# Kernel tuning notes

Hardware: AMD Instinct MI355X
Metric: run time of the kernel (lower is better)

The kernel has to match this reference:

```python
import jax, jax.numpy as jnp
import numpy as np

DIM = 1024
N_HEADS = 16
N_KV = 4
HEAD_DIM = 64
FFN = 4096
EPS = 1e-6
B, S = 2, 2048
ROPE_BASE = 10000.0


def rmsnorm(x, w, eps=EPS):
    ms = jnp.mean(jnp.square(x), axis=-1, keepdims=True)
    return x * jax.lax.rsqrt(ms + eps) * w


def apply_rotary(x, cos, sin):
    # x: [B,H,S,hd]; cos/sin: [S, hd//2] -> broadcast over B,H
    half = x.shape[-1] // 2
    x1, x2 = x[..., :half], x[..., half:]
    c = cos[None, None, :, :]
    s = sin[None, None, :, :]
    return jnp.concatenate((x1 * c + x2 * s, x2 * c - x1 * s), axis=-1)


def setup_inputs() -> dict:
    key = jax.random.key(0)
    ks = jax.random.split(key, 10)
    w = lambda k, shp: jax.random.normal(k, shp, dtype=jnp.float32) * 0.02
    pos = jnp.arange(S, dtype=jnp.float32)
    inv_freq = 1.0 / (ROPE_BASE ** (jnp.arange(0, HEAD_DIM // 2, dtype=jnp.float32) / (HEAD_DIM // 2)))
    ang = pos[:, None] * inv_freq[None, :]
    return {
        "x": jax.random.normal(ks[0], (B, S, DIM), dtype=jnp.float32),
        "w_norm1": jnp.ones((DIM,), jnp.float32),
        "wq": w(ks[1], (DIM, N_HEADS * HEAD_DIM)),
        "wk": w(ks[2], (DIM, N_KV * HEAD_DIM)),
        "wv": w(ks[3], (DIM, N_KV * HEAD_DIM)),
        "wo": w(ks[4], (N_HEADS * HEAD_DIM, DIM)),
        "attn_scale": jnp.ones((DIM,), jnp.float32),
        "w_norm2": jnp.ones((DIM,), jnp.float32),
        "wg": w(ks[5], (DIM, FFN)),
        "wu": w(ks[6], (DIM, FFN)),
        "wd": w(ks[7], (FFN, DIM)),
        "mlp_scale": jnp.ones((DIM,), jnp.float32),
        "cos": jnp.cos(ang),
        "sin": jnp.sin(ang),
    }


def block_forward(x, w_norm1, wq, wk, wv, wo, attn_scale, w_norm2, wg, wu, wd, mlp_scale, cos, sin):
    b, s, d = x.shape
    # ---- attention sub-block (pre-norm, RoPE, causal GQA SDPA, scaled residual) ----
    xn = rmsnorm(x, w_norm1)
    q = (xn @ wq).reshape(b, s, N_HEADS, HEAD_DIM).transpose(0, 2, 1, 3)  # [B,H,S,hd]
    k = (xn @ wk).reshape(b, s, N_KV, HEAD_DIM).transpose(0, 2, 1, 3)    # [B,KV,S,hd]
    v = (xn @ wv).reshape(b, s, N_KV, HEAD_DIM).transpose(0, 2, 1, 3)
    q = apply_rotary(q, cos, sin)
    k = apply_rotary(k, cos, sin)
    rep = N_HEADS // N_KV
    k = jnp.repeat(k, rep, axis=1)  # GQA expand -> [B,H,S,hd]
    v = jnp.repeat(v, rep, axis=1)
    scale = 1.0 / np.sqrt(HEAD_DIM)
    scores = jnp.einsum("bhqd,bhkd->bhqk", q, k) * scale
    causal = jnp.tril(jnp.ones((s, s), dtype=bool))
    scores = jnp.where(causal[None, None], scores, jnp.finfo(scores.dtype).min)
    probs = jax.nn.softmax(scores, axis=-1)
    attn = jnp.einsum("bhqk,bhkd->bhqd", probs, v)
    attn = attn.transpose(0, 2, 1, 3).reshape(b, s, N_HEADS * HEAD_DIM)
    x = x + (attn @ wo) * attn_scale[None, None, :]
    # ---- MLP sub-block (pre-norm, fused gate/up SwiGLU, down proj, scaled residual) ----
    xn2 = rmsnorm(x, w_norm2)
    hidden = jax.nn.silu(xn2 @ wg) * (xn2 @ wu)  # SwiGLU
    x = x + (hidden @ wd) * mlp_scale[None, None, :]
    return x


def reference(x, w_norm1, wq, wk, wv, wo, attn_scale, w_norm2, wg, wu, wd, mlp_scale, cos, sin):
    return block_forward(x, w_norm1, wq, wk, wv, wo, attn_scale, w_norm2, wg, wu, wd, mlp_scale, cos, sin)
```

## Files before the change

kernel.cpp:

```cpp
#include <hip/hip_runtime.h>
#include <hip/hip_bf16.h>
#include <cstdint>

typedef unsigned short u16;
typedef unsigned int u32;
typedef __attribute__((ext_vector_type(4))) float f32x4;
typedef __attribute__((ext_vector_type(16))) float f32x16;
typedef __attribute__((ext_vector_type(8))) __bf16 bf16x8;

#define NH 16
#define NKV 4
#define SEQ 2048
#define NTOK 4096

__device__ inline u16 f2bf(float f) {
  return __builtin_bit_cast(u16, __float2bfloat16(f));
}
__device__ inline float bf2f(u16 u) {
  return __bfloat162float(__builtin_bit_cast(__hip_bfloat16, u));
}
__device__ inline u32 pk2(float a, float b) {
  return (u32)f2bf(a) | ((u32)f2bf(b) << 16);
}

#define GLDS(gp, lp) __builtin_amdgcn_global_load_lds( \
    (__attribute__((address_space(1))) void*)(gp), \
    (__attribute__((address_space(3))) void*)(lp), 16, 0, 0)

#define VMCNT0 asm volatile("s_waitcnt vmcnt(0)" ::: "memory")

__global__ __launch_bounds__(256) void rmsnorm_kernel(
    const float* __restrict__ x, const float* __restrict__ w,
    u16* __restrict__ out) {
  int row = blockIdx.x;
  int tid = threadIdx.x;
  const float4 v = reinterpret_cast<const float4*>(x + (size_t)row * 1024)[tid];
  float ss = v.x * v.x + v.y * v.y + v.z * v.z + v.w * v.w;
#pragma unroll
  for (int off = 32; off; off >>= 1) ss += __shfl_xor(ss, off);
  __shared__ float red[4];
  int lane = tid & 63, wid = tid >> 6;
  if (lane == 0) red[wid] = ss;
  __syncthreads();
  float tot = red[0] + red[1] + red[2] + red[3];
  float r = rsqrtf(tot * (1.0f / 1024.0f) + 1e-6f);
  const float4 wv = reinterpret_cast<const float4*>(w)[tid];
  ushort4 o;
  o.x = f2bf(v.x * r * wv.x);
  o.y = f2bf(v.y * r * wv.y);
  o.z = f2bf(v.z * r * wv.z);
  o.w = f2bf(v.w * r * wv.w);
  reinterpret_cast<ushort4*>(out + (size_t)row * 1024)[tid] = o;
}

__global__ __launch_bounds__(256) void transpose_cast_kernel(
    const float* __restrict__ src, u16* __restrict__ dst, int K, int N) {
  __shared__ float tile[32][33];
  int n0 = blockIdx.x * 32, k0 = blockIdx.y * 32;
  int tx = threadIdx.x & 31, ty = threadIdx.x >> 5;
#pragma unroll
  for (int i = 0; i < 4; i++)
    tile[ty + i * 8][tx] = src[(size_t)(k0 + ty + i * 8) * N + n0 + tx];
  __syncthreads();
#pragma unroll
  for (int i = 0; i < 4; i++)
    dst[(size_t)(n0 + ty + i * 8) * K + k0 + tx] = f2bf(tile[tx][ty + i * 8]);
}

template <int EP>
__device__ inline void epi_store(float v, size_t idx, int col,
                                 float* __restrict__ outf,
                                 const float* __restrict__ res,
                                 const float* __restrict__ scale,
                                 u16* __restrict__ outb) {
  if (EP == 0) {
    outf[idx] = v;
  } else if (EP == 1) {
    outf[idx] = res[idx] + v * scale[col];
  } else if (EP == 2) {
    outb[idx] = f2bf(v / (1.0f + __expf(-v)));
  } else {
    outb[idx] = f2bf(bf2f(outb[idx]) * v);
  }
}

template <int EP>
__global__ __launch_bounds__(512, 1) void gemmA(
    const u16* __restrict__ A, const u16* __restrict__ Bt,
    int M, int N, int K,
    float* __restrict__ outf, const float* __restrict__ res,
    const float* __restrict__ scale, u16* __restrict__ outb) {
  __shared__ u16 SA[2][256 * 64];
  __shared__ u16 SB[2][256 * 64];
  const int tid = threadIdx.x, lane = tid & 63, w = tid >> 6;
  const int wr = w >> 2, wc = w & 3;
  const int lg = lane >> 4, lc = lane & 15, cx = lc & 7;

  const int nbn = N >> 8;
  const int r8 = blockIdx.x & 7, j = blockIdx.x >> 3;
  const int bm = (((r8 >> 1) << 2) + (j & 3)) << 8;
  const int bn = ((r8 & 1) * (nbn >> 1) + (j >> 2)) << 8;

  const int swrow = lane >> 3;
  const int swcol = (lane & 7) ^ swrow;
  const u16* gA = A + (size_t)(bm + w * 16 + swrow) * K + swcol * 8;
  const u16* gB = Bt + (size_t)(bn + w * 16 + swrow) * K + swcol * 8;

  const int NT = K >> 6;
  f32x4 acc[8][4] = {};

#define SGA(T_) do { int sl_ = (T_) & 1; size_t ko_ = (size_t)(T_) * 64; \
    GLDS(gA + ko_,                    &SA[sl_][(w * 16) * 64]); \
    GLDS(gA + ko_ + (size_t)8 * K,    &SA[sl_][(w * 16 + 8) * 64]); \
    GLDS(gA + ko_ + (size_t)128 * K,  &SA[sl_][(128 + w * 16) * 64]); \
    GLDS(gA + ko_ + (size_t)136 * K,  &SA[sl_][(136 + w * 16) * 64]); } while (0)
#define SGB(T_) do { int sl_ = (T_) & 1; size_t ko_ = (size_t)(T_) * 64; \
    GLDS(gB + ko_,                    &SB[sl_][(w * 16) * 64]); \
    GLDS(gB + ko_ + (size_t)8 * K,    &SB[sl_][(w * 16 + 8) * 64]); \
    GLDS(gB + ko_ + (size_t)128 * K,  &SB[sl_][(128 + w * 16) * 64]); \
    GLDS(gB + ko_ + (size_t)136 * K,  &SB[sl_][(136 + w * 16) * 64]); } while (0)

  SGA(0);
  SGB(0);
  VMCNT0;
  __builtin_amdgcn_s_barrier();

  for (int t = 0; t < NT; ++t) {
    const u16* sa = &SA[t & 1][0];
    const u16* sb = &SB[t & 1][0];
    const bool more = (t + 1 < NT);

    bf16x8 bfr[4][2];
#pragma unroll
    for (int n = 0; n < 4; n++) {
      const int row = wc * 64 + n * 16 + lc;
#pragma unroll
      for (int ks = 0; ks < 2; ks++)
        bfr[n][ks] = *reinterpret_cast<const bf16x8*>(
            &sb[row * 64 + ((((ks << 2) | lg) ^ cx) << 3)]);
    }
    bf16x8 afr[4][2];
#pragma unroll
    for (int i = 0; i < 4; i++) {
      const int row = wr * 128 + i * 16 + lc;
#pragma unroll
      for (int ks = 0; ks < 2; ks++)
        afr[i][ks] = *reinterpret_cast<const bf16x8*>(
            &sa[row * 64 + ((((ks << 2) | lg) ^ cx) << 3)]);
    }
    if (more) SGA(t + 1);
    __builtin_amdgcn_s_setprio(1);
#pragma unroll
    for (int i = 0; i < 4; i++)
#pragma unroll
      for (int n = 0; n < 4; n++) {
        acc[i][n] = __builtin_amdgcn_mfma_f32_16x16x32_bf16(afr[i][0], bfr[n][0], acc[i][n], 0, 0, 0);
        acc[i][n] = __builtin_amdgcn_mfma_f32_16x16x32_bf16(afr[i][1], bfr[n][1], acc[i][n], 0, 0, 0);
      }
    __builtin_amdgcn_s_setprio(0);
#pragma unroll
    for (int i = 0; i < 4; i++) {
      const int row = wr * 128 + 64 + i * 16 + lc;
#pragma unroll
      for (int ks = 0; ks < 2; ks++)
        afr[i][ks] = *reinterpret_cast<const bf16x8*>(
            &sa[row * 64 + ((((ks << 2) | lg) ^ cx) << 3)]);
    }
    if (more) SGB(t + 1);
    __builtin_amdgcn_s_setprio(1);
#pragma unroll
    for (int i = 0; i < 4; i++)
#pragma unroll
      for (int n = 0; n < 4; n++) {
        acc[4 + i][n] = __builtin_amdgcn_mfma_f32_16x16x32_bf16(afr[i][0], bfr[n][0], acc[4 + i][n], 0, 0, 0);
        acc[4 + i][n] = __builtin_amdgcn_mfma_f32_16x16x32_bf16(afr[i][1], bfr[n][1], acc[4 + i][n], 0, 0, 0);
      }
    __builtin_amdgcn_s_setprio(0);
    VMCNT0;
    __builtin_amdgcn_s_barrier();
  }
#undef SGA
#undef SGB

#pragma unroll
  for (int mi = 0; mi < 8; mi++)
#pragma unroll
    for (int ni = 0; ni < 4; ni++)
#pragma unroll
      for (int rg = 0; rg < 4; rg++) {
        const int row = bm + wr * 128 + mi * 16 + lg * 4 + rg;
        const int col = bn + wc * 64 + ni * 16 + lc;
        epi_store<EP>(acc[mi][ni][rg], (size_t)row * N + col, col, outf, res, scale, outb);
      }
}

template <int EP>
__global__ __launch_bounds__(256, 1) void gemmB(
    const u16* __restrict__ A, const u16* __restrict__ Bt,
    int M, int N, int K,
    float* __restrict__ outf, const float* __restrict__ res,
    const float* __restrict__ scale, u16* __restrict__ outb) {
  __shared__ u16 SA[2][128 * 64];
  __shared__ u16 SB[2][128 * 64];
  const int tid = threadIdx.x, lane = tid & 63, w = tid >> 6;
  const int wr = w >> 1, wc = w & 1;
  const int lg = lane >> 4, lc = lane & 15, cx = lc & 7;

  const int r8 = blockIdx.x & 7, j = blockIdx.x >> 3;
  const int bm = ((r8 << 2) + (j & 3)) << 7;
  const int bn = (j >> 2) << 7;

  const int swrow = lane >> 3;
  const int swcol = (lane & 7) ^ swrow;
  const u16* gA = A + (size_t)(bm + w * 32 + swrow) * K + swcol * 8;
  const u16* gB = Bt + (size_t)(bn + w * 32 + swrow) * K + swcol * 8;

  const int NT = K >> 6;
  f32x4 acc[4][4] = {};

#define SG2(T_) do { int sl_ = (T_) & 1; size_t ko_ = (size_t)(T_) * 64; \
    GLDS(gA + ko_,                   &SA[sl_][(w * 32) * 64]); \
    GLDS(gA + ko_ + (size_t)8 * K,   &SA[sl_][(w * 32 + 8) * 64]); \
    GLDS(gA + ko_ + (size_t)16 * K,  &SA[sl_][(w * 32 + 16) * 64]); \
    GLDS(gA + ko_ + (size_t)24 * K,  &SA[sl_][(w * 32 + 24) * 64]); \
    GLDS(gB + ko_,                   &SB[sl_][(w * 32) * 64]); \
    GLDS(gB + ko_ + (size_t)8 * K,   &SB[sl_][(w * 32 + 8) * 64]); \
    GLDS(gB + ko_ + (size_t)16 * K,  &SB[sl_][(w * 32 + 16) * 64]); \
    GLDS(gB + ko_ + (size_t)24 * K,  &SB[sl_][(w * 32 + 24) * 64]); } while (0)

  SG2(0);
  VMCNT0;
  __builtin_amdgcn_s_barrier();

  for (int t = 0; t < NT; ++t) {
    const u16* sa = &SA[t & 1][0];
    const u16* sb = &SB[t & 1][0];
    const bool more = (t + 1 < NT);

    bf16x8 bfr[4][2], afr[4][2];
#pragma unroll
    for (int n = 0; n < 4; n++) {
      const int row = wc * 64 + n * 16 + lc;
#pragma unroll
      for (int ks = 0; ks < 2; ks++)
        bfr[n][ks] = *reinterpret_cast<const bf16x8*>(
            &sb[row * 64 + ((((ks << 2) | lg) ^ cx) << 3)]);
    }
#pragma unroll
    for (int i = 0; i < 4; i++) {
      const int row = wr * 64 + i * 16 + lc;
#pragma unroll
      for (int ks = 0; ks < 2; ks++)
        afr[i][ks] = *reinterpret_cast<const bf16x8*>(
            &sa[row * 64 + ((((ks << 2) | lg) ^ cx) << 3)]);
    }
    if (more) SG2(t + 1);
    __builtin_amdgcn_s_setprio(1);
#pragma unroll
    for (int i = 0; i < 4; i++)
#pragma unroll
      for (int n = 0; n < 4; n++) {
        acc[i][n] = __builtin_amdgcn_mfma_f32_16x16x32_bf16(afr[i][0], bfr[n][0], acc[i][n], 0, 0, 0);
        acc[i][n] = __builtin_amdgcn_mfma_f32_16x16x32_bf16(afr[i][1], bfr[n][1], acc[i][n], 0, 0, 0);
      }
    __builtin_amdgcn_s_setprio(0);
    VMCNT0;
    __builtin_amdgcn_s_barrier();
  }
#undef SG2

#pragma unroll
  for (int mi = 0; mi < 4; mi++)
#pragma unroll
    for (int ni = 0; ni < 4; ni++)
#pragma unroll
      for (int rg = 0; rg < 4; rg++) {
        const int row = bm + wr * 64 + mi * 16 + lg * 4 + rg;
        const int col = bn + wc * 64 + ni * 16 + lc;
        epi_store<EP>(acc[mi][ni][rg], (size_t)row * N + col, col, outf, res, scale, outb);
      }
}

__global__ __launch_bounds__(256) void rope_kernel(
    const float* __restrict__ qkv, const float* __restrict__ cosb,
    const float* __restrict__ sinb, u16* __restrict__ qr, u16* __restrict__ kr) {
  int idx = blockIdx.x * 256 + threadIdx.x;
  int d = idx & 31;
  int t = idx >> 5;
  int head = t % 20;
  int bs = t / 20;
  int s = bs & (SEQ - 1);
  int b = bs >> 11;
  const float* row = qkv + (size_t)bs * 1536;
  float c = cosb[s * 32 + d], sn = sinb[s * 32 + d];
  const float QSC = 0.18033688011112042f;
  float x1, x2;
  if (head < 16) {
    x1 = row[head * 64 + d];
    x2 = row[head * 64 + d + 32];
    size_t o = ((size_t)(b * NH + head) * SEQ + s) * 64 + d;
    qr[o] = f2bf((x1 * c + x2 * sn) * QSC);
    qr[o + 32] = f2bf((x2 * c - x1 * sn) * QSC);
  } else {
    int kh = head - 16;
    x1 = row[1024 + kh * 64 + d];
    x2 = row[1024 + kh * 64 + d + 32];
    size_t o = ((size_t)(b * NKV + kh) * SEQ + s) * 64 + d;
    kr[o] = f2bf(x1 * c + x2 * sn);
    kr[o + 32] = f2bf(x2 * c - x1 * sn);
  }
}

__global__ __launch_bounds__(256) void vtrans_kernel(
    const float* __restrict__ qkv, u16* __restrict__ vt) {
  int blk = blockIdx.x;
  int st = blk & 31; blk >>= 5;
  int kvh = blk & 3; blk >>= 2;
  int b = blk;
  __shared__ u16 tile[64][65];
  int tx = threadIdx.x & 63;
  int ty = threadIdx.x >> 6;
  int s0 = st * 64;
#pragma unroll
  for (int i = 0; i < 16; i++) {
    int sl = i * 4 + ty;
    tile[sl][tx] = f2bf(qkv[(size_t)(b * SEQ + s0 + sl) * 1536 + 1280 + kvh * 64 + tx]);
  }
  __syncthreads();
  size_t vbase = (size_t)(b * NKV + kvh) * 64 * SEQ;
#pragma unroll
  for (int i = 0; i < 16; i++) {
    int dd = i * 4 + ty;
    vt[vbase + (size_t)dd * SEQ + s0 + tx] = tile[tx][dd];
  }
}

__global__ __launch_bounds__(512, 1) void attn_kernel(
    const u16* __restrict__ qr, const u16* __restrict__ kr,
    const u16* __restrict__ vt, u16* __restrict__ out) {
  __shared__ u16 Ks[2][64 * 64];
  __shared__ u16 Vs[2][64 * 64];

  const int n = blockIdx.x;
  const int g = n & 7;
  const int b = g >> 2, kvh = g & 3;
  const int h = kvh * 4 + ((n >> 3) & 3);
  const int i = n >> 5;

  const int tid = threadIdx.x;
  const int lane = tid & 63, w = tid >> 6;
  const int l31 = lane & 31, hi = lane >> 5;

  const int q0w = i * 256 + w * 32;
  const int qg = q0w + l31;
  const int nt = 4 * i + 4;

  bf16x8 qf[4];
  {
    const u16* qp = qr + ((size_t)(b * NH + h) * SEQ + qg) * 64 + 8 * hi;
#pragma unroll
    for (int c = 0; c < 4; c++)
      qf[c] = *reinterpret_cast<const bf16x8*>(qp + 16 * c);
  }
  VMCNT0;

  const int srow = lane >> 3;
  const int scw = ((lane & 7) ^ srow) << 3;
  const u16* ksrc = kr + (size_t)(b * NKV + kvh) * SEQ * 64 + (size_t)(w * 8 + srow) * 64 + scw;
  const u16* vsrc = vt + ((size_t)(b * NKV + kvh) * 64 + w * 8 + srow) * SEQ + scw;

#define STAGEA(bufi, t) do { \
    GLDS(ksrc + (size_t)(t) * 64 * 64, &Ks[bufi][(w * 8) * 64]); \
    GLDS(vsrc + (size_t)(t) * 64,      &Vs[bufi][(w * 8) * 64]); \
  } while (0)

  STAGEA(0, 0);

  float mm = -1e30f, ll = 0.0f;
  f32x16 oacc[2] = {};

  int buf = 0;
  for (int t = 0; t < nt; ++t) {
    if (t + 1 < nt) {
      STAGEA(buf ^ 1, t + 1);
      asm volatile("s_waitcnt vmcnt(2)" ::: "memory");
    } else {
      VMCNT0;
    }
    __builtin_amdgcn_s_barrier();
    __builtin_amdgcn_sched_barrier(0);

    const int c0 = t * 64;
    if (c0 <= q0w + 31) {
      f32x16 sc[2] = {};
      __builtin_amdgcn_s_setprio(1);
#pragma unroll
      for (int a = 0; a < 2; a++) {
        const int row = a * 32 + l31;
#pragma unroll
        for (int c = 0; c < 4; c++) {
          bf16x8 kf = *reinterpret_cast<const bf16x8*>(
              &Ks[buf][row * 64 + (((2 * c + hi) ^ (row & 7)) << 3)]);
          sc[a] = __builtin_amdgcn_mfma_f32_32x32x16_bf16(kf, qf[c], sc[a], 0, 0, 0);
        }
      }
      __builtin_amdgcn_s_setprio(0);

      bf16x8 vf[2][4];
#pragma unroll
      for (int dch = 0; dch < 2; dch++) {
        const int row = dch * 32 + l31;
#pragma unroll
        for (int c = 0; c < 4; c++)
          vf[dch][c] = *reinterpret_cast<const bf16x8*>(
              &Vs[buf][row * 64 + (((2 * c + hi) ^ (row & 7)) << 3)]);
      }

      if (c0 + 63 > q0w) {
#pragma unroll
        for (int a = 0; a < 2; a++)
#pragma unroll
          for (int r = 0; r < 16; r++) {
            const int key = c0 + 32 * a + (r & 3) + 8 * (r >> 2) + 4 * hi;
            if (key > qg) sc[a][r] = -1e30f;
          }
      }

      float mx = -1e30f;
#pragma unroll
      for (int a = 0; a < 2; a++)
#pragma unroll
        for (int r = 0; r < 16; r++) mx = fmaxf(mx, sc[a][r]);
      mx = fmaxf(mx, __shfl_xor(mx, 32));

      if (!__all(mx - mm <= 11.5f)) {
        float mn = fmaxf(mm, mx);
        float al = exp2f(mm - mn);
        mm = mn;
        ll *= al;
#pragma unroll
        for (int r = 0; r < 16; r++) {
          float arr = __shfl(al, (r & 3) + 8 * (r >> 2) + 4 * hi);
          oacc[0][r] *= arr;
          oacc[1][r] *= arr;
        }
      }

      float rs = 0.0f;
#pragma unroll
      for (int a = 0; a < 2; a++)
#pragma unroll
        for (int r = 0; r < 16; r++) {
          float p = exp2f(sc[a][r] - mm);
          sc[a][r] = p;
          rs += p;
        }
      rs += __shfl_xor(rs, 32);
      ll += rs;

      bf16x8 pa[4];
#pragma unroll
      for (int c = 0; c < 4; c++) {
        const int a = c >> 1;
        const int bb = 8 * (c & 1);
        u32 A0 = pk2(sc[a][bb + 0], sc[a][bb + 1]);
        u32 A1 = pk2(sc[a][bb + 2], sc[a][bb + 3]);
        u32 B0 = pk2(sc[a][bb + 4], sc[a][bb + 5]);
        u32 B1 = pk2(sc[a][bb + 6], sc[a][bb + 7]);
        u32 s0 = hi ? A0 : B0;
        u32 s1 = hi ? A1 : B1;
        u32 r0 = (u32)__shfl_xor((int)s0, 32);
        u32 r1 = (u32)__shfl_xor((int)s1, 32);
        u32 w0 = hi ? r0 : A0;
        u32 w1 = hi ? r1 : A1;
        u32 w2 = hi ? B0 : r0;
        u32 w3 = hi ? B1 : r1;
        uint4 pw;
        pw.x = w0; pw.y = w1; pw.z = w2; pw.w = w3;
        pa[c] = __builtin_bit_cast(bf16x8, pw);
      }

      __builtin_amdgcn_s_setprio(1);
#pragma unroll
      for (int c = 0; c < 4; c++) {
        oacc[0] = __builtin_amdgcn_mfma_f32_32x32x16_bf16(pa[c], vf[0][c], oacc[0], 0, 0, 0);
        oacc[1] = __builtin_amdgcn_mfma_f32_32x32x16_bf16(pa[c], vf[1][c], oacc[1], 0, 0, 0);
      }
      __builtin_amdgcn_s_setprio(0);
    }
    asm volatile("s_waitcnt lgkmcnt(0)" ::: "memory");
    __builtin_amdgcn_s_barrier();
    __builtin_amdgcn_sched_barrier(0);
    buf ^= 1;
  }
#undef STAGEA

  const float li = 1.0f / ll;
#pragma unroll
  for (int r = 0; r < 16; r++) {
    const int qloc = (r & 3) + 8 * (r >> 2) + 4 * hi;
    float liq = __shfl(li, qloc);
    const int q = q0w + qloc;
    u16* orow = out + (size_t)(b * SEQ + q) * 1024 + h * 64 + l31;
    orow[0] = f2bf(oacc[0][r] * liq);
    orow[32] = f2bf(oacc[1][r] * liq);
  }
}

extern "C" void kernel_launch(void* const* d_in, const int* in_sizes, int n_in,
                              void* d_out, int out_size, void* d_ws, size_t ws_size,
                              hipStream_t stream) {
  const float* x = (const float*)d_in[0];
  const float* w_norm1 = (const float*)d_in[1];
  const float* wq = (const float*)d_in[2];
  const float* wk = (const float*)d_in[3];
  const float* wv = (const float*)d_in[4];
  const float* wo = (const float*)d_in[5];
  const float* attn_scale = (const float*)d_in[6];
  const float* w_norm2 = (const float*)d_in[7];
  const float* wg = (const float*)d_in[8];
  const float* wu = (const float*)d_in[9];
  const float* wd = (const float*)d_in[10];
  const float* mlp_scale = (const float*)d_in[11];
  const float* cosb = (const float*)d_in[12];
  const float* sinb = (const float*)d_in[13];
  float* out = (float*)d_out;

  char* ws = (char*)d_ws;
  u16* wqkv_t = (u16*)(ws + 0);
  u16* wo_t = (u16*)(ws + 3145728);
  u16* wg_t = (u16*)(ws + 5242880);
  u16* wu_t = (u16*)(ws + 13631488);
  u16* wd_t = (u16*)(ws + 22020096);
  u16* xn = (u16*)(ws + 30408704);
  float* qkv = (float*)(ws + 38797312);
  u16* attn_o = (u16*)(ws + 38797312);
  float* x1 = (float*)(ws + 47185920);
  u16* q_rope = (u16*)(ws + 63963136);
  u16* k_rope = (u16*)(ws + 72351744);
  u16* vt = (u16*)(ws + 74448896);
  u16* hbuf = (u16*)(ws + 63963136);

  dim3 tb(256);
  transpose_cast_kernel<<<dim3(32, 32), tb, 0, stream>>>(wq, wqkv_t, 1024, 1024);
  transpose_cast_kernel<<<dim3(8, 32), tb, 0, stream>>>(wk, wqkv_t + (size_t)1024 * 1024, 1024, 256);
  transpose_cast_kernel<<<dim3(8, 32), tb, 0, stream>>>(wv, wqkv_t + (size_t)1280 * 1024, 1024, 256);
  transpose_cast_kernel<<<dim3(32, 32), tb, 0, stream>>>(wo, wo_t, 1024, 1024);
  transpose_cast_kernel<<<dim3(128, 32), tb, 0, stream>>>(wg, wg_t, 1024, 4096);
  transpose_cast_kernel<<<dim3(128, 32), tb, 0, stream>>>(wu, wu_t, 1024, 4096);
  transpose_cast_kernel<<<dim3(32, 128), tb, 0, stream>>>(wd, wd_t, 4096, 1024);

  rmsnorm_kernel<<<4096, tb, 0, stream>>>(x, w_norm1, xn);
  gemmB<0><<<dim3(384), dim3(256), 0, stream>>>(xn, wqkv_t, 4096, 1536, 1024, qkv, nullptr, nullptr, nullptr);
  rope_kernel<<<10240, tb, 0, stream>>>(qkv, cosb, sinb, q_rope, k_rope);
  vtrans_kernel<<<2 * 4 * 32, tb, 0, stream>>>(qkv, vt);
  attn_kernel<<<256, dim3(512), 0, stream>>>(q_rope, k_rope, vt, attn_o);
  gemmB<1><<<dim3(256), dim3(256), 0, stream>>>(attn_o, wo_t, 4096, 1024, 1024, x1, x, attn_scale, nullptr);
  rmsnorm_kernel<<<4096, tb, 0, stream>>>(x1, w_norm2, xn);
  gemmA<2><<<dim3(256), dim3(512), 0, stream>>>(xn, wg_t, 4096, 4096, 1024, nullptr, nullptr, nullptr, hbuf);
  gemmA<3><<<dim3(256), dim3(512), 0, stream>>>(xn, wu_t, 4096, 4096, 1024, nullptr, nullptr, nullptr, hbuf);
  gemmB<1><<<dim3(256), dim3(256), 0, stream>>>(hbuf, wd_t, 4096, 1024, 4096, out, x1, mlp_scale, nullptr);
}
```

Baseline: 303.8 us.

## Pair mirrored causal query blocks per workgroup and load K/V directly to registers

The attention kernel now assigns each 256-thread workgroup two mirrored 128-row query blocks (j and 15-j), so every block does about the same amount of causal work. K and V fragments are loaded from global memory straight into registers, which removes the double-buffered LDS staging and its barriers. The K/V tiles are shared between the two query sets, but each wave now issues its own global loads with no cross-wave reuse through LDS. Register pressure also rises because two sets of accumulators are kept live.

```diff
diff --git a/kernel.cpp b/kernel.cpp
--- a/kernel.cpp
+++ b/kernel.cpp
@@ -335,176 +335,163 @@
   }
 }
 
-__global__ __launch_bounds__(512, 1) void attn_kernel(
+__global__ __launch_bounds__(256, 1) void attn_kernel(
     const u16* __restrict__ qr, const u16* __restrict__ kr,
     const u16* __restrict__ vt, u16* __restrict__ out) {
-  __shared__ u16 Ks[2][64 * 64];
-  __shared__ u16 Vs[2][64 * 64];
-
   const int n = blockIdx.x;
   const int g = n & 7;
   const int b = g >> 2, kvh = g & 3;
   const int h = kvh * 4 + ((n >> 3) & 3);
-  const int i = n >> 5;
+  const int j = n >> 5;
 
   const int tid = threadIdx.x;
   const int lane = tid & 63, w = tid >> 6;
   const int l31 = lane & 31, hi = lane >> 5;
 
-  const int q0w = i * 256 + w * 32;
-  const int qg = q0w + l31;
-  const int nt = 4 * i + 4;
-
-  bf16x8 qf[4];
+  const int qA0 = j * 128 + w * 32;
+  const int qB0 = (15 - j) * 128 + w * 32;
+  const int qgA = qA0 + l31, qgB = qB0 + l31;
+  const int ntA = (qA0 >> 6) + 1;
+  const int ntB = (qB0 >> 6) + 1;
+
+  bf16x8 qfA[4], qfB[4];
   {
-    const u16* qp = qr + ((size_t)(b * NH + h) * SEQ + qg) * 64 + 8 * hi;
-#pragma unroll
-    for (int c = 0; c < 4; c++)
-      qf[c] = *reinterpret_cast<const bf16x8*>(qp + 16 * c);
-  }
-  VMCNT0;
-
-  const int srow = lane >> 3;
-  const int scw = ((lane & 7) ^ srow) << 3;
-  const u16* ksrc = kr + (size_t)(b * NKV + kvh) * SEQ * 64 + (size_t)(w * 8 + srow) * 64 + scw;
-  const u16* vsrc = vt + ((size_t)(b * NKV + kvh) * 64 + w * 8 + srow) * SEQ + scw;
-
-#define STAGEA(bufi, t) do { \
-    GLDS(ksrc + (size_t)(t) * 64 * 64, &Ks[bufi][(w * 8) * 64]); \
-    GLDS(vsrc + (size_t)(t) * 64,      &Vs[bufi][(w * 8) * 64]); \
+    const u16* qpA = qr + ((size_t)(b * NH + h) * SEQ + qgA) * 64 + 8 * hi;
+    const u16* qpB = qr + ((size_t)(b * NH + h) * SEQ + qgB) * 64 + 8 * hi;
+#pragma unroll
+    for (int c = 0; c < 4; c++) {
+      qfA[c] = *reinterpret_cast<const bf16x8*>(qpA + 16 * c);
+      qfB[c] = *reinterpret_cast<const bf16x8*>(qpB + 16 * c);
+    }
+  }
+
+  const u16* kl = kr + (size_t)(b * NKV + kvh) * SEQ * 64 + (size_t)l31 * 64 + 8 * hi;
+  const u16* vl = vt + (size_t)(b * NKV + kvh) * 64 * SEQ + (size_t)l31 * SEQ + 8 * hi;
+
+  float mmA = -1e30f, llA = 0.0f, mmB = -1e30f, llB = 0.0f;
+  f32x16 oA0 = {}, oA1 = {}, oB0 = {}, oB1 = {};
+
+  for (int t = 0; t < ntB; ++t) {
+    const int c0 = t * 64;
+    const bool doA = (t < ntA);
+
+    bf16x8 kf[2][4];
+#pragma unroll
+    for (int a = 0; a < 2; a++)
+#pragma unroll
+      for (int c = 0; c < 4; c++)
+        kf[a][c] = *reinterpret_cast<const bf16x8*>(kl + (size_t)(c0 + 32 * a) * 64 + 16 * c);
+
+    bf16x8 vf[2][4];
+#pragma unroll
+    for (int dch = 0; dch < 2; dch++)
+#pragma unroll
+      for (int c = 0; c < 4; c++)
+        vf[dch][c] = *reinterpret_cast<const bf16x8*>(vl + (size_t)dch * 32 * SEQ + c0 + 16 * c);
+
+    f32x16 scA0 = {}, scA1 = {}, scB0 = {}, scB1 = {};
+#pragma unroll
+    for (int c = 0; c < 4; c++) {
+      scB0 = __builtin_amdgcn_mfma_f32_32x32x16_bf16(kf[0][c], qfB[c], scB0, 0, 0, 0);
+      scB1 = __builtin_amdgcn_mfma_f32_32x32x16_bf16(kf[1][c], qfB[c], scB1, 0, 0, 0);
+    }
+    if (doA) {
+#pragma unroll
+      for (int c = 0; c < 4; c++) {
+        scA0 = __builtin_amdgcn_mfma_f32_32x32x16_bf16(kf[0][c], qfA[c], scA0, 0, 0, 0);
+        scA1 = __builtin_amdgcn_mfma_f32_32x32x16_bf16(kf[1][c], qfA[c], scA1, 0, 0, 0);
+      }
+    }
+
+#define SOFTMAX_PV(scx0, scx1, qg_, q0_, mm_, ll_, o0_, o1_)                 \
+    do {                                                                     \
+      if (c0 + 63 > (q0_)) {                                                 \
+        _Pragma("unroll") for (int r = 0; r < 16; r++) {                     \
+          const int krow = (r & 3) + 8 * (r >> 2) + 4 * hi;                  \
+          if (c0 + krow > (qg_)) scx0[r] = -1e30f;                           \
+          if (c0 + 32 + krow > (qg_)) scx1[r] = -1e30f;                      \
+        }                                                                    \
+      }                                                                      \
+      float mx = -1e30f;                                                     \
+      _Pragma("unroll") for (int r = 0; r < 16; r++) {                       \
+        mx = fmaxf(mx, scx0[r]);                                             \
+        mx = fmaxf(mx, scx1[r]);                                             \
+      }                                                                      \
+      mx = fmaxf(mx, __shfl_xor(mx, 32));                                    \
+      if (!__all(mx - (mm_) <= 11.5f)) {                                     \
+        float mn = fmaxf((mm_), mx);                                         \
+        float al = exp2f((mm_) - mn);                                        \
+        (mm_) = mn;                                                          \
+        (ll_) *= al;                                                         \
+        _Pragma("unroll") for (int r = 0; r < 16; r++) {                     \
+          float arr = __shfl(al, (r & 3) + 8 * (r >> 2) + 4 * hi);           \
+          o0_[r] *= arr;                                                     \
+          o1_[r] *= arr;                                                     \
+        }                                                                    \
+      }                                                                      \
+      float rs = 0.0f;                                                       \
+      _Pragma("unroll") for (int r = 0; r < 16; r++) {                       \
+        float p0 = exp2f(scx0[r] - (mm_));                                   \
+        float p1 = exp2f(scx1[r] - (mm_));                                   \
+        scx0[r] = p0;                                                        \
+        scx1[r] = p1;                                                        \
+        rs += p0 + p1;                                                       \
+      }                                                                      \
+      rs += __shfl_xor(rs, 32);                                              \
+      (ll_) += rs;                                                           \
+      bf16x8 pa[4];                                                          \
+      _Pragma("unroll") for (int c = 0; c < 4; c++) {                        \
+        const int bb = 8 * (c & 1);                                          \
+        u32 A0, A1, B0, B1;                                                  \
+        if (c < 2) {                                                         \
+          A0 = pk2(scx0[bb + 0], scx0[bb + 1]);                              \
+          A1 = pk2(scx0[bb + 2], scx0[bb + 3]);                              \
+          B0 = pk2(scx0[bb + 4], scx0[bb + 5]);                              \
+          B1 = pk2(scx0[bb + 6], scx0[bb + 7]);                              \
+        } else {                                                             \
+          A0 = pk2(scx1[bb + 0], scx1[bb + 1]);                              \
+          A1 = pk2(scx1[bb + 2], scx1[bb + 3]);                              \
+          B0 = pk2(scx1[bb + 4], scx1[bb + 5]);                              \
+          B1 = pk2(scx1[bb + 6], scx1[bb + 7]);                              \
+        }                                                                    \
+        u32 s0 = hi ? A0 : B0;                                               \
+        u32 s1 = hi ? A1 : B1;                                               \
+        u32 r0 = (u32)__shfl_xor((int)s0, 32);                               \
+        u32 r1 = (u32)__shfl_xor((int)s1, 32);                               \
+        uint4 pw;                                                            \
+        pw.x = hi ? r0 : A0;                                                 \
+        pw.y = hi ? r1 : A1;                                                 \
+        pw.z = hi ? B0 : r0;                                                 \
+        pw.w = hi ? B1 : r1;                                                 \
+        pa[c] = __builtin_bit_cast(bf16x8, pw);                              \
+      }                                                                      \
+      _Pragma("unroll") for (int c = 0; c < 4; c++) {                        \
+        o0_ = __builtin_amdgcn_mfma_f32_32x32x16_bf16(pa[c], vf[0][c], o0_, 0, 0, 0); \
+        o1_ = __builtin_amdgcn_mfma_f32_32x32x16_bf16(pa[c], vf[1][c], o1_, 0, 0, 0); \
+      }                                                                      \
+    } while (0)
+
+    SOFTMAX_PV(scB0, scB1, qgB, qB0, mmB, llB, oB0, oB1);
+    if (doA) SOFTMAX_PV(scA0, scA1, qgA, qA0, mmA, llA, oA0, oA1);
+#undef SOFTMAX_PV
+  }
+
+#define WRITE_SET(q0_, ll_, o0_, o1_)                                        \
+  do {                                                                       \
+    const float li = 1.0f / (ll_);                                           \
+    _Pragma("unroll") for (int r = 0; r < 16; r++) {                         \
+      const int qloc = (r & 3) + 8 * (r >> 2) + 4 * hi;                      \
+      float liq = __shfl(li, qloc);                                          \
+      const int q = (q0_) + qloc;                                            \
+      u16* orow = out + (size_t)(b * SEQ + q) * 1024 + h * 64 + l31;         \
+      orow[0] = f2bf(o0_[r] * liq);                                          \
+      orow[32] = f2bf(o1_[r] * liq);                                         \
+    }                                                                        \
   } while (0)
 
-  STAGEA(0, 0);
-
-  float mm = -1e30f, ll = 0.0f;
-  f32x16 oacc[2] = {};
-
-  int buf = 0;
-  for (int t = 0; t < nt; ++t) {
-    if (t + 1 < nt) {
-      STAGEA(buf ^ 1, t + 1);
-      asm volatile("s_waitcnt vmcnt(2)" ::: "memory");
-    } else {
-      VMCNT0;
-    }
-    __builtin_amdgcn_s_barrier();
-    __builtin_amdgcn_sched_barrier(0);
-
-    const int c0 = t * 64;
-    if (c0 <= q0w + 31) {
-      f32x16 sc[2] = {};
-      __builtin_amdgcn_s_setprio(1);
-#pragma unroll
-      for (int a = 0; a < 2; a++) {
-        const int row = a * 32 + l31;
-#pragma unroll
-        for (int c = 0; c < 4; c++) {
-          bf16x8 kf = *reinterpret_cast<const bf16x8*>(
-              &Ks[buf][row * 64 + (((2 * c + hi) ^ (row & 7)) << 3)]);
-          sc[a] = __builtin_amdgcn_mfma_f32_32x32x16_bf16(kf, qf[c], sc[a], 0, 0, 0);
-        }
-      }
-      __builtin_amdgcn_s_setprio(0);
-
-      bf16x8 vf[2][4];
-#pragma unroll
-      for (int dch = 0; dch < 2; dch++) {
-        const int row = dch * 32 + l31;
-#pragma unroll
-        for (int c = 0; c < 4; c++)
-          vf[dch][c] = *reinterpret_cast<const bf16x8*>(
-              &Vs[buf][row * 64 + (((2 * c + hi) ^ (row & 7)) << 3)]);
-      }
-
-      if (c0 + 63 > q0w) {
-#pragma unroll
-        for (int a = 0; a < 2; a++)
-#pragma unroll
-          for (int r = 0; r < 16; r++) {
-            const int key = c0 + 32 * a + (r & 3) + 8 * (r >> 2) + 4 * hi;
-            if (key > qg) sc[a][r] = -1e30f;
-          }
-      }
-
-      float mx = -1e30f;
-#pragma unroll
-      for (int a = 0; a < 2; a++)
-#pragma unroll
-        for (int r = 0; r < 16; r++) mx = fmaxf(mx, sc[a][r]);
-      mx = fmaxf(mx, __shfl_xor(mx, 32));
-
-      if (!__all(mx - mm <= 11.5f)) {
-        float mn = fmaxf(mm, mx);
-        float al = exp2f(mm - mn);
-        mm = mn;
-        ll *= al;
-#pragma unroll
-        for (int r = 0; r < 16; r++) {
-          float arr = __shfl(al, (r & 3) + 8 * (r >> 2) + 4 * hi);
-          oacc[0][r] *= arr;
-          oacc[1][r] *= arr;
-        }
-      }
-
-      float rs = 0.0f;
-#pragma unroll
-      for (int a = 0; a < 2; a++)
-#pragma unroll
-        for (int r = 0; r < 16; r++) {
-          float p = exp2f(sc[a][r] - mm);
-          sc[a][r] = p;
-          rs += p;
-        }
-      rs += __shfl_xor(rs, 32);
-      ll += rs;
-
-      bf16x8 pa[4];
-#pragma unroll
-      for (int c = 0; c < 4; c++) {
-        const int a = c >> 1;
-        const int bb = 8 * (c & 1);
-        u32 A0 = pk2(sc[a][bb + 0], sc[a][bb + 1]);
-        u32 A1 = pk2(sc[a][bb + 2], sc[a][bb + 3]);
-        u32 B0 = pk2(sc[a][bb + 4], sc[a][bb + 5]);
-        u32 B1 = pk2(sc[a][bb + 6], sc[a][bb + 7]);
-        u32 s0 = hi ? A0 : B0;
-        u32 s1 = hi ? A1 : B1;
-        u32 r0 = (u32)__shfl_xor((int)s0, 32);
-        u32 r1 = (u32)__shfl_xor((int)s1, 32);
-        u32 w0 = hi ? r0 : A0;
-        u32 w1 = hi ? r1 : A1;
-        u32 w2 = hi ? B0 : r0;
-        u32 w3 = hi ? B1 : r1;
-        uint4 pw;
-        pw.x = w0; pw.y = w1; pw.z = w2; pw.w = w3;
-        pa[c] = __builtin_bit_cast(bf16x8, pw);
-      }
-
-      __builtin_amdgcn_s_setprio(1);
-#pragma unroll
-      for (int c = 0; c < 4; c++) {
-        oacc[0] = __builtin_amdgcn_mfma_f32_32x32x16_bf16(pa[c], vf[0][c], oacc[0], 0, 0, 0);
-        oacc[1] = __builtin_amdgcn_mfma_f32_32x32x16_bf16(pa[c], vf[1][c], oacc[1], 0, 0, 0);
-      }
-      __builtin_amdgcn_s_setprio(0);
-    }
-    asm volatile("s_waitcnt lgkmcnt(0)" ::: "memory");
-    __builtin_amdgcn_s_barrier();
-    __builtin_amdgcn_sched_barrier(0);
-    buf ^= 1;
-  }
-#undef STAGEA
-
-  const float li = 1.0f / ll;
-#pragma unroll
-  for (int r = 0; r < 16; r++) {
-    const int qloc = (r & 3) + 8 * (r >> 2) + 4 * hi;
-    float liq = __shfl(li, qloc);
-    const int q = q0w + qloc;
-    u16* orow = out + (size_t)(b * SEQ + q) * 1024 + h * 64 + l31;
-    orow[0] = f2bf(oacc[0][r] * liq);
-    orow[32] = f2bf(oacc[1][r] * liq);
-  }
+  WRITE_SET(qA0, llA, oA0, oA1);
+  WRITE_SET(qB0, llB, oB0, oB1);
+#undef WRITE_SET
 }
 
 extern "C" void kernel_launch(void* const* d_in, const int* in_sizes, int n_in,
@@ -554,7 +541,7 @@
   gemmB<0><<<dim3(384), dim3(256), 0, stream>>>(xn, wqkv_t, 4096, 1536, 1024, qkv, nullptr, nullptr, nullptr);
   rope_kernel<<<10240, tb, 0, stream>>>(qkv, cosb, sinb, q_rope, k_rope);
   vtrans_kernel<<<2 * 4 * 32, tb, 0, stream>>>(qkv, vt);
-  attn_kernel<<<256, dim3(512), 0, stream>>>(q_rope, k_rope, vt, attn_o);
+  attn_kernel<<<256, dim3(256), 0, stream>>>(q_rope, k_rope, vt, attn_o);
   gemmB<1><<<dim3(256), dim3(256), 0, stream>>>(attn_o, wo_t, 4096, 1024, 1024, x1, x, attn_scale, nullptr);
   rmsnorm_kernel<<<4096, tb, 0, stream>>>(x1, w_norm2, xn);
   gemmA<2><<<dim3(256), dim3(512), 0, stream>>>(xn, wg_t, 4096, 4096, 1024, nullptr, nullptr, nullptr, hbuf);
```

Measured after the change: 291.7 us. 4.0% less time.

## Rebalance causal attention by pairing low/high query blocks with split-KV merge

Applied to the files above, without the earlier changes.

Each workgroup now pairs a low and a mirrored high 128-row query block so every block does the same causal work. Warps 4-7 take the first half of the high block's key range, and the partial max, sum and output are merged through shared memory. K and V fragments are now read straight from global memory instead of through double-buffered LDS staging, and launch bounds allow two blocks per CU. This targets causal load imbalance and the per-tile barriers, at the cost of uncoalesced, L2-dependent global loads and no explicit prefetch.

```diff
diff --git a/kernel.cpp b/kernel.cpp
--- a/kernel.cpp
+++ b/kernel.cpp
@@ -335,175 +335,210 @@
   }
 }
 
-__global__ __launch_bounds__(512, 1) void attn_kernel(
+__device__ __forceinline__ void attn_span(
+    const u16* __restrict__ kl, const u16* __restrict__ vl,
+    const bf16x8 qf[4], int t0, int t1, int q0, int hi, int l31,
+    float& mm, float& ll, f32x16& o0, f32x16& o1) {
+  const int qg = q0 + l31;
+  for (int t = t0; t < t1; ++t) {
+    const int c0 = t * 64;
+    bf16x8 kf[2][4];
+#pragma unroll
+    for (int a = 0; a < 2; a++)
+#pragma unroll
+      for (int c = 0; c < 4; c++)
+        kf[a][c] = *reinterpret_cast<const bf16x8*>(kl + (size_t)(c0 + 32 * a) * 64 + 16 * c);
+    bf16x8 vf[2][4];
+#pragma unroll
+    for (int dch = 0; dch < 2; dch++)
+#pragma unroll
+      for (int c = 0; c < 4; c++)
+        vf[dch][c] = *reinterpret_cast<const bf16x8*>(vl + (size_t)dch * 32 * SEQ + c0 + 16 * c);
+
+    f32x16 sc0 = {}, sc1 = {};
+#pragma unroll
+    for (int c = 0; c < 4; c++) {
+      sc0 = __builtin_amdgcn_mfma_f32_32x32x16_bf16(kf[0][c], qf[c], sc0, 0, 0, 0);
+      sc1 = __builtin_amdgcn_mfma_f32_32x32x16_bf16(kf[1][c], qf[c], sc1, 0, 0, 0);
+    }
+
+    if (c0 + 63 > q0) {
+#pragma unroll
+      for (int r = 0; r < 16; r++) {
+        const int krow = (r & 3) + 8 * (r >> 2) + 4 * hi;
+        if (c0 + krow > qg) sc0[r] = -1e30f;
+        if (c0 + 32 + krow > qg) sc1[r] = -1e30f;
+      }
+    }
+
+    float mx = -1e30f;
+#pragma unroll
+    for (int r = 0; r < 16; r++) {
+      mx = fmaxf(mx, sc0[r]);
+      mx = fmaxf(mx, sc1[r]);
+    }
+    mx = fmaxf(mx, __shfl_xor(mx, 32));
+
+    if (!__all(mx - mm <= 11.5f)) {
+      float mn = fmaxf(mm, mx);
+      float al = exp2f(mm - mn);
+      mm = mn;
+      ll *= al;
+#pragma unroll
+      for (int r = 0; r < 16; r++) {
+        float arr = __shfl(al, (r & 3) + 8 * (r >> 2) + 4 * hi);
+        o0[r] *= arr;
+        o1[r] *= arr;
+      }
+    }
+
+    float rs = 0.0f;
+#pragma unroll
+    for (int r = 0; r < 16; r++) {
+      float p0 = exp2f(sc0[r] - mm);
+      float p1 = exp2f(sc1[r] - mm);
+      sc0[r] = p0;
+      sc1[r] = p1;
+      rs += p0 + p1;
+    }
+    rs += __shfl_xor(rs, 32);
+    ll += rs;
+
+    bf16x8 pa[4];
+#pragma unroll
+    for (int c = 0; c < 4; c++) {
+      const int bb = 8 * (c & 1);
+      u32 A0, A1, B0, B1;
+      if (c < 2) {
+        A0 = pk2(sc0[bb + 0], sc0[bb + 1]);
+        A1 = pk2(sc0[bb + 2], sc0[bb + 3]);
+        B0 = pk2(sc0[bb + 4], sc0[bb + 5]);
+        B1 = pk2(sc0[bb + 6], sc0[bb + 7]);
+      } else {
+        A0 = pk2(sc1[bb + 0], sc1[bb + 1]);
+        A1 = pk2(sc1[bb + 2], sc1[bb + 3]);
+        B0 = pk2(sc1[bb + 4], sc1[bb + 5]);
+        B1 = pk2(sc1[bb + 6], sc1[bb + 7]);
+      }
+      u32 s0 = hi ? A0 : B0;
+      u32 s1 = hi ? A1 : B1;
+      u32 r0 = (u32)__shfl_xor((int)s0, 32);
+      u32 r1 = (u32)__shfl_xor((int)s1, 32);
+      uint4 pw;
+      pw.x = hi ? r0 : A0;
+      pw.y = hi ? r1 : A1;
+      pw.z = hi ? B0 : r0;
+      pw.w = hi ? B1 : r1;
+      pa[c] = __builtin_bit_cast(bf16x8, pw);
+    }
+#pragma unroll
+    for (int c = 0; c < 4; c++) {
+      o0 = __builtin_amdgcn_mfma_f32_32x32x16_bf16(pa[c], vf[0][c], o0, 0, 0, 0);
+      o1 = __builtin_amdgcn_mfma_f32_32x32x16_bf16(pa[c], vf[1][c], o1, 0, 0, 0);
+    }
+  }
+}
+
+__global__ __launch_bounds__(512, 2) void attn_kernel(
     const u16* __restrict__ qr, const u16* __restrict__ kr,
     const u16* __restrict__ vt, u16* __restrict__ out) {
-  __shared__ u16 Ks[2][64 * 64];
-  __shared__ u16 Vs[2][64 * 64];
+  __shared__ float pO[4][32][64];
+  __shared__ float pM[4][32];
+  __shared__ float pL[4][32];
 
   const int n = blockIdx.x;
   const int g = n & 7;
   const int b = g >> 2, kvh = g & 3;
   const int h = kvh * 4 + ((n >> 3) & 3);
-  const int i = n >> 5;
+  const int j = n >> 5;
 
   const int tid = threadIdx.x;
   const int lane = tid & 63, w = tid >> 6;
   const int l31 = lane & 31, hi = lane >> 5;
-
-  const int q0w = i * 256 + w * 32;
-  const int qg = q0w + l31;
-  const int nt = 4 * i + 4;
-
-  bf16x8 qf[4];
-  {
-    const u16* qp = qr + ((size_t)(b * NH + h) * SEQ + qg) * 64 + 8 * hi;
-#pragma unroll
-    for (int c = 0; c < 4; c++)
-      qf[c] = *reinterpret_cast<const bf16x8*>(qp + 16 * c);
-  }
-  VMCNT0;
-
-  const int srow = lane >> 3;
-  const int scw = ((lane & 7) ^ srow) << 3;
-  const u16* ksrc = kr + (size_t)(b * NKV + kvh) * SEQ * 64 + (size_t)(w * 8 + srow) * 64 + scw;
-  const u16* vsrc = vt + ((size_t)(b * NKV + kvh) * 64 + w * 8 + srow) * SEQ + scw;
-
-#define STAGEA(bufi, t) do { \
-    GLDS(ksrc + (size_t)(t) * 64 * 64, &Ks[bufi][(w * 8) * 64]); \
-    GLDS(vsrc + (size_t)(t) * 64,      &Vs[bufi][(w * 8) * 64]); \
-  } while (0)
-
-  STAGEA(0, 0);
-
-  float mm = -1e30f, ll = 0.0f;
-  f32x16 oacc[2] = {};
-
-  int buf = 0;
-  for (int t = 0; t < nt; ++t) {
-    if (t + 1 < nt) {
-      STAGEA(buf ^ 1, t + 1);
-      asm volatile("s_waitcnt vmcnt(2)" ::: "memory");
-    } else {
-      VMCNT0;
-    }
-    __builtin_amdgcn_s_barrier();
-    __builtin_amdgcn_sched_barrier(0);
-
-    const int c0 = t * 64;
-    if (c0 <= q0w + 31) {
-      f32x16 sc[2] = {};
-      __builtin_amdgcn_s_setprio(1);
-#pragma unroll
-      for (int a = 0; a < 2; a++) {
-        const int row = a * 32 + l31;
-#pragma unroll
-        for (int c = 0; c < 4; c++) {
-          bf16x8 kf = *reinterpret_cast<const bf16x8*>(
-              &Ks[buf][row * 64 + (((2 * c + hi) ^ (row & 7)) << 3)]);
-          sc[a] = __builtin_amdgcn_mfma_f32_32x32x16_bf16(kf, qf[c], sc[a], 0, 0, 0);
-        }
-      }
-      __builtin_amdgcn_s_setprio(0);
-
-      bf16x8 vf[2][4];
-#pragma unroll
-      for (int dch = 0; dch < 2; dch++) {
-        const int row = dch * 32 + l31;
-#pragma unroll
-        for (int c = 0; c < 4; c++)
-          vf[dch][c] = *reinterpret_cast<const bf16x8*>(
-              &Vs[buf][row * 64 + (((2 * c + hi) ^ (row & 7)) << 3)]);
-      }
-
-      if (c0 + 63 > q0w) {
-#pragma unroll
-        for (int a = 0; a < 2; a++)
-#pragma unroll
-          for (int r = 0; r < 16; r++) {
-            const int key = c0 + 32 * a + (r & 3) + 8 * (r >> 2) + 4 * hi;
-            if (key > qg) sc[a][r] = -1e30f;
-          }
-      }
-
-      float mx = -1e30f;
-#pragma unroll
-      for (int a = 0; a < 2; a++)
-#pragma unroll
-        for (int r = 0; r < 16; r++) mx = fmaxf(mx, sc[a][r]);
-      mx = fmaxf(mx, __shfl_xor(mx, 32));
-
-      if (!__all(mx - mm <= 11.5f)) {
-        float mn = fmaxf(mm, mx);
-        float al = exp2f(mm - mn);
-        mm = mn;
-        ll *= al;
-#pragma unroll
-        for (int r = 0; r < 16; r++) {
-          float arr = __shfl(al, (r & 3) + 8 * (r >> 2) + 4 * hi);
-          oacc[0][r] *= arr;
-          oacc[1][r] *= arr;
-        }
-      }
-
-      float rs = 0.0f;
-#pragma unroll
-      for (int a = 0; a < 2; a++)
-#pragma unroll
-        for (int r = 0; r < 16; r++) {
-          float p = exp2f(sc[a][r] - mm);
-          sc[a][r] = p;
-          rs += p;
-        }
-      rs += __shfl_xor(rs, 32);
-      ll += rs;
-
-      bf16x8 pa[4];
-#pragma unroll
-      for (int c = 0; c < 4; c++) {
-        const int a = c >> 1;
-        const int bb = 8 * (c & 1);
-        u32 A0 = pk2(sc[a][bb + 0], sc[a][bb + 1]);
-        u32 A1 = pk2(sc[a][bb + 2], sc[a][bb + 3]);
-        u32 B0 = pk2(sc[a][bb + 4], sc[a][bb + 5]);
-        u32 B1 = pk2(sc[a][bb + 6], sc[a][bb + 7]);
-        u32 s0 = hi ? A0 : B0;
-        u32 s1 = hi ? A1 : B1;
-        u32 r0 = (u32)__shfl_xor((int)s0, 32);
-        u32 r1 = (u32)__shfl_xor((int)s1, 32);
-        u32 w0 = hi ? r0 : A0;
-        u32 w1 = hi ? r1 : A1;
-        u32 w2 = hi ? B0 : r0;
-        u32 w3 = hi ? B1 : r1;
-        uint4 pw;
-        pw.x = w0; pw.y = w1; pw.z = w2; pw.w = w3;
-        pa[c] = __builtin_bit_cast(bf16x8, pw);
-      }
-
-      __builtin_amdgcn_s_setprio(1);
-#pragma unroll
-      for (int c = 0; c < 4; c++) {
-        oacc[0] = __builtin_amdgcn_mfma_f32_32x32x16_bf16(pa[c], vf[0][c], oacc[0], 0, 0, 0);
-        oacc[1] = __builtin_amdgcn_mfma_f32_32x32x16_bf16(pa[c], vf[1][c], oacc[1], 0, 0, 0);
-      }
-      __builtin_amdgcn_s_setprio(0);
-    }
-    asm volatile("s_waitcnt lgkmcnt(0)" ::: "memory");
-    __builtin_amdgcn_s_barrier();
-    __builtin_amdgcn_sched_barrier(0);
-    buf ^= 1;
-  }
-#undef STAGEA
-
-  const float li = 1.0f / ll;
-#pragma unroll
-  for (int r = 0; r < 16; r++) {
-    const int qloc = (r & 3) + 8 * (r >> 2) + 4 * hi;
-    float liq = __shfl(li, qloc);
-    const int q = q0w + qloc;
-    u16* orow = out + (size_t)(b * SEQ + q) * 1024 + h * 64 + l31;
-    orow[0] = f2bf(oacc[0][r] * liq);
-    orow[32] = f2bf(oacc[1][r] * liq);
+  const int sub = w & 3, role = w >> 2;
+
+  const int qL0 = j * 128 + sub * 32;
+  const int qH0 = (15 - j) * 128 + sub * 32;
+  const int TL = (qL0 >> 6) + 1;
+  const int TH = (qH0 >> 6) + 1;
+  const int S = (TL + TH) >> 1;
+
+  const u16* kl = kr + (size_t)(b * NKV + kvh) * SEQ * 64 + (size_t)l31 * 64 + 8 * hi;
+  const u16* vl = vt + (size_t)(b * NKV + kvh) * 64 * SEQ + (size_t)l31 * SEQ + 8 * hi;
+  const u16* qbase = qr + (size_t)(b * NH + h) * SEQ * 64 + 8 * hi;
+
+  float mmH = -1e30f, llH = 0.0f;
+  f32x16 oH0 = {}, oH1 = {};
+
+  if (role == 0) {
+    bf16x8 qf[4];
+    {
+      const u16* qp = qbase + (size_t)(qL0 + l31) * 64;
+#pragma unroll
+      for (int c = 0; c < 4; c++) qf[c] = *reinterpret_cast<const bf16x8*>(qp + 16 * c);
+    }
+    float mm = -1e30f, ll = 0.0f;
+    f32x16 o0 = {}, o1 = {};
+    attn_span(kl, vl, qf, 0, TL, qL0, hi, l31, mm, ll, o0, o1);
+    {
+      const float li = 1.0f / ll;
+#pragma unroll
+      for (int r = 0; r < 16; r++) {
+        const int qloc = (r & 3) + 8 * (r >> 2) + 4 * hi;
+        float liq = __shfl(li, qloc);
+        u16* orow = out + (size_t)(b * SEQ + qL0 + qloc) * 1024 + h * 64 + l31;
+        orow[0] = f2bf(o0[r] * liq);
+        orow[32] = f2bf(o1[r] * liq);
+      }
+    }
+    bf16x8 qfH[4];
+    {
+      const u16* qp = qbase + (size_t)(qH0 + l31) * 64;
+#pragma unroll
+      for (int c = 0; c < 4; c++) qfH[c] = *reinterpret_cast<const bf16x8*>(qp + 16 * c);
+    }
+    attn_span(kl, vl, qfH, S, TH, qH0, hi, l31, mmH, llH, oH0, oH1);
+  } else {
+    bf16x8 qfH[4];
+    {
+      const u16* qp = qbase + (size_t)(qH0 + l31) * 64;
+#pragma unroll
+      for (int c = 0; c < 4; c++) qfH[c] = *reinterpret_cast<const bf16x8*>(qp + 16 * c);
+    }
+    attn_span(kl, vl, qfH, 0, S, qH0, hi, l31, mmH, llH, oH0, oH1);
+#pragma unroll
+    for (int r = 0; r < 16; r++) {
+      const int qloc = (r & 3) + 8 * (r >> 2) + 4 * hi;
+      pO[sub][qloc][l31] = oH0[r];
+      pO[sub][qloc][32 + l31] = oH1[r];
+    }
+    if (hi == 0) {
+      pM[sub][l31] = mmH;
+      pL[sub][l31] = llH;
+    }
+  }
+
+  __syncthreads();
+
+  if (role == 0) {
+    const float m1 = pM[sub][l31];
+    const float l1 = pL[sub][l31];
+    const float mN = fmaxf(mmH, m1);
+    const float a0 = exp2f(mmH - mN);
+    const float a1 = exp2f(m1 - mN);
+    const float li = 1.0f / (llH * a0 + l1 * a1);
+#pragma unroll
+    for (int r = 0; r < 16; r++) {
+      const int qloc = (r & 3) + 8 * (r >> 2) + 4 * hi;
+      float a0q = __shfl(a0, qloc);
+      float a1q = __shfl(a1, qloc);
+      float liq = __shfl(li, qloc);
+      float v0 = oH0[r] * a0q + pO[sub][qloc][l31] * a1q;
+      float v1 = oH1[r] * a0q + pO[sub][qloc][32 + l31] * a1q;
+      u16* orow = out + (size_t)(b * SEQ + qH0 + qloc) * 1024 + h * 64 + l31;
+      orow[0] = f2bf(v0 * liq);
+      orow[32] = f2bf(v1 * liq);
+    }
   }
 }
 
```

New measurement: 291.5 us. 1.04x faster.
